# Kernel optimization log

Measured on AMD Instinct MI355X. Metric: run time of the kernel, lower is better.

The kernel has to match this reference:

```python
import jax, jax.numpy as jnp
import numpy as np

EPS = 1e-5

def layernorm(x, g, b):
    mu = jnp.mean(x, axis=-1, keepdims=True)
    var = jnp.mean(jnp.square(x - mu), axis=-1, keepdims=True)
    return (x - mu) * jax.lax.rsqrt(var + EPS) * g + b

def setup_inputs() -> dict:
    key = jax.random.key(0)
    ks = jax.random.split(key, 12)
    B, T, C, H = 4, 2048, 1024, 8
    Dh = C // H          # 128
    Dff = 4 * C          # 4096
    s = 0.02
    return {
        "x":     jax.random.normal(ks[0], (B, T, C), jnp.float32),
        "wq":    jax.random.normal(ks[1], (H, C, Dh), jnp.float32) * s,
        "wk":    jax.random.normal(ks[2], (H, C, Dh), jnp.float32) * s,
        "wv":    jax.random.normal(ks[3], (H, C, Dh), jnp.float32) * s,
        "w1":    jax.random.normal(ks[4], (C, Dff), jnp.float32) * s,
        "b1":    jnp.zeros((Dff,), jnp.float32),
        "w2":    jax.random.normal(ks[5], (Dff, C), jnp.float32) * s,
        "b2":    jnp.zeros((C,), jnp.float32),
        "ln1_g": jnp.ones((C,), jnp.float32),
        "ln1_b": jnp.zeros((C,), jnp.float32),
        "ln2_g": jnp.ones((C,), jnp.float32),
        "ln2_b": jnp.zeros((C,), jnp.float32),
    }

def reference(x, wq, wk, wv, w1, b1, w2, b2, ln1_g, ln1_b, ln2_g, ln2_b):
    B, T, C = x.shape
    H, _, Dh = wq.shape
    # --- multi-head self-attention (pre-LN) ---
    h = layernorm(x, ln1_g, ln1_b)
    q = jnp.einsum("btc,hcd->bhtd", h, wq)
    k = jnp.einsum("btc,hcd->bhtd", h, wk)
    v = jnp.einsum("btc,hcd->bhtd", h, wv)
    # NOTE: original multiplies by sqrt(head_size) (not divide) -- kept faithful
    scores = jnp.einsum("bhtd,bhsd->bhts", q, k) * (Dh ** 0.5)
    attn = jax.nn.softmax(scores, axis=-1)
    # dropout(p=0.2) treated as identity (eval mode)
    o = jnp.einsum("bhts,bhsd->bhtd", attn, v)
    # concat heads along last dim: head h fills contiguous slice
    o = o.transpose(0, 2, 1, 3).reshape(B, T, H * Dh)
    x = x + o  # no output projection in original module
    # --- feed-forward (pre-LN) ---
    h2 = layernorm(x, ln2_g, ln2_b)
    ff = jax.nn.relu(h2 @ w1 + b1) @ w2 + b2
    return x + ff
```

## Files before the change

kernel.cpp:

```cpp
#include <hip/hip_runtime.h>
#include <hip/hip_bf16.h>
#include <math.h>

#define B_   4
#define T_   2048
#define C_   1024
#define H_   8
#define DH   128
#define DFF  4096
#define M_   (B_*T_)

typedef __attribute__((ext_vector_type(8))) short bf16x8;
typedef __attribute__((ext_vector_type(4))) float f32x4;
typedef __attribute__((ext_vector_type(2))) unsigned int u32x2;

#define SC2 16.32223094f

__device__ __forceinline__ unsigned short f2bf(float x) {
  union { float f; unsigned u; } v; v.f = x;
  return (unsigned short)((v.u + 0x7fffu + ((v.u >> 16) & 1u)) >> 16);
}
__device__ __forceinline__ float bf2f(unsigned short h) {
  union { unsigned u; float f; } v; v.u = ((unsigned)h) << 16; return v.f;
}

__device__ __forceinline__ f32x4 mfma_bf16(bf16x8 a, bf16x8 b, f32x4 c) {
  return __builtin_amdgcn_mfma_f32_16x16x32_bf16(a, b, c, 0, 0, 0);
}

__device__ __forceinline__ void gll16(const void* g, void* l) {
  __builtin_amdgcn_global_load_lds((const __attribute__((address_space(1))) void*)g,
                                   (__attribute__((address_space(3))) void*)l,
                                   16, 0, 0);
}

__global__ __launch_bounds__(256) void ln_kernel(const float* __restrict__ in,
                                                 const float* __restrict__ g,
                                                 const float* __restrict__ bb,
                                                 unsigned short* __restrict__ h_hi,
                                                 unsigned short* __restrict__ h_lo) {
  __shared__ float red[8];
  const int row = blockIdx.x;
  const int tid = threadIdx.x;
  const float* p = in + (size_t)row * C_;
  const float4 xv = *(const float4*)(p + (tid << 2));
  float s  = xv.x + xv.y + xv.z + xv.w;
  float sq = xv.x*xv.x + xv.y*xv.y + xv.z*xv.z + xv.w*xv.w;
  #pragma unroll
  for (int off = 32; off > 0; off >>= 1) {
    s  += __shfl_xor(s, off);
    sq += __shfl_xor(sq, off);
  }
  if ((tid & 63) == 0) { red[(tid >> 6) * 2] = s; red[(tid >> 6) * 2 + 1] = sq; }
  __syncthreads();
  s  = red[0] + red[2] + red[4] + red[6];
  sq = red[1] + red[3] + red[5] + red[7];
  const float mu  = s * (1.0f / C_);
  const float var = sq * (1.0f / C_) - mu * mu;
  const float rs  = rsqrtf(var + 1e-5f);
  const float4 gv = *(const float4*)(g  + (tid << 2));
  const float4 bv = *(const float4*)(bb + (tid << 2));
  float ov[4];
  ov[0] = (xv.x - mu) * rs * gv.x + bv.x;
  ov[1] = (xv.y - mu) * rs * gv.y + bv.y;
  ov[2] = (xv.z - mu) * rs * gv.z + bv.z;
  ov[3] = (xv.w - mu) * rs * gv.w + bv.w;
  ushort4 hv, lv;
  unsigned short* hp = (unsigned short*)&hv;
  unsigned short* lp = (unsigned short*)&lv;
  #pragma unroll
  for (int j = 0; j < 4; ++j) {
    hp[j] = f2bf(ov[j]);
    lp[j] = f2bf(ov[j] - bf2f(hp[j]));
  }
  *(ushort4*)(h_hi + (size_t)row * C_ + (tid << 2)) = hv;
  *(ushort4*)(h_lo + (size_t)row * C_ + (tid << 2)) = lv;
}

__global__ __launch_bounds__(256) void cvt_t_kernel(const float* __restrict__ in,
                                                    unsigned short* __restrict__ out,
                                                    int R, int CC) {
  __shared__ float tile[32][33];
  const int r0 = blockIdx.y << 5, c0 = blockIdx.x << 5;
  const int tr = threadIdx.x >> 3, tc4 = (threadIdx.x & 7) << 2;
  const float4 vv = *(const float4*)(in + (size_t)(r0 + tr) * CC + c0 + tc4);
  tile[tr][tc4+0] = vv.x; tile[tr][tc4+1] = vv.y;
  tile[tr][tc4+2] = vv.z; tile[tr][tc4+3] = vv.w;
  __syncthreads();
  ushort4 o;
  o.x = f2bf(tile[tc4+0][tr]); o.y = f2bf(tile[tc4+1][tr]);
  o.z = f2bf(tile[tc4+2][tr]); o.w = f2bf(tile[tc4+3][tr]);
  *(ushort4*)(out + (size_t)(c0 + tr) * R + r0 + tc4) = o;
}

__global__ __launch_bounds__(256) void cvt_qkv_kernel(const float* __restrict__ wq,
                                                      const float* __restrict__ wk,
                                                      const float* __restrict__ wv,
                                                      unsigned short* __restrict__ wt_hi,
                                                      unsigned short* __restrict__ wt_lo) {
  const int z = blockIdx.z;
  const int which = z >> 3, head = z & 7;
  const float* in = (which == 0 ? wq : (which == 1 ? wk : wv)) + (size_t)head * C_ * DH;
  unsigned short* oh = wt_hi + (size_t)z * DH * C_;
  unsigned short* ol = wt_lo + (size_t)z * DH * C_;
  __shared__ float tile[32][33];
  const int r0 = blockIdx.y << 5, c0 = blockIdx.x << 5;
  const int tr = threadIdx.x >> 3, tc4 = (threadIdx.x & 7) << 2;
  const float4 vv = *(const float4*)(in + (size_t)(r0 + tr) * DH + c0 + tc4);
  tile[tr][tc4+0] = vv.x; tile[tr][tc4+1] = vv.y;
  tile[tr][tc4+2] = vv.z; tile[tr][tc4+3] = vv.w;
  __syncthreads();
  ushort4 hv, lv;
  unsigned short* hp = (unsigned short*)&hv;
  unsigned short* lp = (unsigned short*)&lv;
  #pragma unroll
  for (int j = 0; j < 4; ++j) {
    const float val = tile[tc4+j][tr];
    hp[j] = f2bf(val);
    lp[j] = f2bf(val - bf2f(hp[j]));
  }
  *(ushort4*)(oh + (size_t)(c0 + tr) * C_ + r0 + tc4) = hv;
  *(ushort4*)(ol + (size_t)(c0 + tr) * C_ + r0 + tc4) = lv;
}


__device__ __forceinline__ void gemm128_split3(
    const unsigned short* __restrict__ Ah, const unsigned short* __restrict__ Al,
    int lda,
    const unsigned short* __restrict__ Bh, const unsigned short* __restrict__ Bl,
    int ldb, int K, f32x4 (&acc)[4][4],
    unsigned short* AhS, unsigned short* AlS,
    unsigned short* BhS, unsigned short* BlS) {
  const int tid  = threadIdx.x;
  const int w    = tid >> 6;
  const int lane = tid & 63;
  const int l15  = lane & 15, quad = lane >> 4;
  const int srow = lane >> 2;
  const int skc  = ((lane & 3) << 3) ^ (((srow >> 1) & 3) << 3);
  const int wm = w & 1, wn = w >> 1;
  const int ro = ((quad ^ ((l15 >> 1) & 3)) << 3);

  for (int k0 = 0; k0 < K; k0 += 32) {
    __syncthreads();
    #pragma unroll
    for (int i = 0; i < 2; ++i) {
      const int seg  = w * 2 + i;
      const int r    = seg * 16 + srow;
      const int lofs = seg * 512 + lane * 8;
      gll16(Ah + (size_t)r * lda + k0 + skc, AhS + lofs);
      gll16(Bh + (size_t)r * ldb + k0 + skc, BhS + lofs);
      gll16(Al + (size_t)r * lda + k0 + skc, AlS + lofs);
      gll16(Bl + (size_t)r * ldb + k0 + skc, BlS + lofs);
    }
    __syncthreads();
    bf16x8 aH[4], bH[4], aL[4], bL[4];
    #pragma unroll
    for (int t = 0; t < 4; ++t) {
      aH[t] = *(const bf16x8*)&AhS[(wm * 64 + t * 16 + l15) * 32 + ro];
      bH[t] = *(const bf16x8*)&BhS[(wn * 64 + t * 16 + l15) * 32 + ro];
      aL[t] = *(const bf16x8*)&AlS[(wm * 64 + t * 16 + l15) * 32 + ro];
      bL[t] = *(const bf16x8*)&BlS[(wn * 64 + t * 16 + l15) * 32 + ro];
    }
    #pragma unroll
    for (int rt = 0; rt < 4; ++rt)
      #pragma unroll
      for (int ct = 0; ct < 4; ++ct) {
        acc[rt][ct] = mfma_bf16(aL[rt], bH[ct], acc[rt][ct]);
        acc[rt][ct] = mfma_bf16(aH[rt], bL[ct], acc[rt][ct]);
        acc[rt][ct] = mfma_bf16(aH[rt], bH[ct], acc[rt][ct]);
      }
  }
}

__device__ __forceinline__ void gemm128_db(
    const unsigned short* __restrict__ Ah, int lda,
    const unsigned short* __restrict__ Bh, int ldb, int K, f32x4 (&acc)[4][4],
    unsigned short (&AS0)[4096], unsigned short (&AS1)[4096],
    unsigned short (&BS0)[4096], unsigned short (&BS1)[4096]) {
  const int tid  = threadIdx.x;
  const int w    = tid >> 6;
  const int lane = tid & 63;
  const int l15  = lane & 15, quad = lane >> 4;
  const int srow = lane >> 2;
  const int skc  = ((lane & 3) << 3) ^ (((srow >> 1) & 3) << 3);
  const int wm = w & 1, wn = w >> 1;
  const int ro = ((quad ^ ((l15 >> 1) & 3)) << 3);
  const int Km = K - 1;

  auto STG = [&](int k0, unsigned short* A, unsigned short* B) {
    #pragma unroll
    for (int i = 0; i < 2; ++i) {
      const int seg  = w * 2 + i;
      const int r    = seg * 16 + srow;
      const int lofs = seg * 512 + lane * 8;
      gll16(Ah + (size_t)r * lda + k0 + skc, A + lofs);
      gll16(Bh + (size_t)r * ldb + k0 + skc, B + lofs);
    }
  };
  auto CMP = [&](const unsigned short* A, const unsigned short* B) {
    bf16x8 aH[4], bH[4];
    #pragma unroll
    for (int t = 0; t < 4; ++t) {
      aH[t] = *(const bf16x8*)&A[(wm * 64 + t * 16 + l15) * 32 + ro];
      bH[t] = *(const bf16x8*)&B[(wn * 64 + t * 16 + l15) * 32 + ro];
    }
    #pragma unroll
    for (int rt = 0; rt < 4; ++rt)
      #pragma unroll
      for (int ct = 0; ct < 4; ++ct)
        acc[rt][ct] = mfma_bf16(aH[rt], bH[ct], acc[rt][ct]);
  };

  STG(0, AS0, BS0);
  for (int k0 = 0; k0 < K; k0 += 64) {
    __syncthreads();
    STG((k0 + 32) & Km, AS1, BS1);
    CMP(AS0, BS0);
    __syncthreads();
    STG((k0 + 64) & Km, AS0, BS0);
    CMP(AS1, BS1);
  }
}

__global__ __launch_bounds__(256) void qkm_kernel(const unsigned short* __restrict__ h_hi,
                                                  const unsigned short* __restrict__ h_lo,
                                                  const unsigned short* __restrict__ wt_hi,
                                                  const unsigned short* __restrict__ wt_lo,
                                                  unsigned short* __restrict__ q_hi,
                                                  unsigned short* __restrict__ q_lo,
                                                  unsigned short* __restrict__ k_hi,
                                                  unsigned short* __restrict__ k_lo) {
  __shared__ __align__(16) unsigned short AhS[4096], AlS[4096];
  __shared__ __align__(16) unsigned short BhS[4096], BlS[4096];
  const int m0 = blockIdx.x << 7;
  const int z  = blockIdx.y;
  const int which = z >> 3, head = z & 7;
  f32x4 acc[4][4];
  #pragma unroll
  for (int i = 0; i < 4; ++i)
    #pragma unroll
    for (int j = 0; j < 4; ++j)
      #pragma unroll
      for (int r = 0; r < 4; ++r) acc[i][j][r] = 0.f;
  gemm128_split3(h_hi + (size_t)m0 * C_, h_lo + (size_t)m0 * C_, C_,
                 wt_hi + (size_t)z * DH * C_, wt_lo + (size_t)z * DH * C_, C_,
                 C_, acc, AhS, AlS, BhS, BlS);
  const int lane = threadIdx.x & 63, w = threadIdx.x >> 6;
  const int l15 = lane & 15, quad = lane >> 4;
  const int wm = w & 1, wn = w >> 1;
  const int bh = (m0 >> 11) * H_ + head;
  const int tbase = (m0 & (T_ - 1)) + wm * 64 + quad * 4;
  if (which == 0) {
    #pragma unroll
    for (int rt = 0; rt < 4; ++rt)
      #pragma unroll
      for (int ct = 0; ct < 4; ++ct) {
        const int d = wn * 64 + ct * 16 + l15;
        #pragma unroll
        for (int r = 0; r < 4; ++r) {
          const int t = tbase + rt * 16 + r;
          const float val = acc[rt][ct][r] * SC2;
          const unsigned short hb = f2bf(val);
          const size_t idx = ((size_t)bh * T_ + t) * DH + d;
          q_hi[idx] = hb;
          q_lo[idx] = f2bf(val - bf2f(hb));
        }
      }
  } else {
    #pragma unroll
    for (int rt = 0; rt < 4; ++rt)
      #pragma unroll
      for (int ct = 0; ct < 4; ++ct) {
        const int d = wn * 64 + ct * 16 + l15;
        #pragma unroll
        for (int r = 0; r < 4; ++r) {
          const int t = tbase + rt * 16 + r;
          const int tt = t & 31;
          const float val = acc[rt][ct][r];
          const unsigned short hb = f2bf(val);
          const size_t idx = (((size_t)bh * 64 + (t >> 5)) * 4 + (d >> 5)) * 1024
                           + (size_t)tt * 32 + ((d & 31) ^ (((tt >> 1) & 3) << 3));
          k_hi[idx] = hb;
          k_lo[idx] = f2bf(val - bf2f(hb));
        }
      }
  }
}

__global__ __launch_bounds__(256) void vm_kernel(const unsigned short* __restrict__ h_hi,
                                                 const unsigned short* __restrict__ wv_hi,
                                                 unsigned short* __restrict__ vimg) {
  __shared__ __align__(16) unsigned short AS0[4096], AS1[4096];
  __shared__ __align__(16) unsigned short BS0[4096], BS1[4096];
  const int m0 = blockIdx.x << 7;
  const int head = blockIdx.y;
  f32x4 acc[4][4];
  #pragma unroll
  for (int i = 0; i < 4; ++i)
    #pragma unroll
    for (int j = 0; j < 4; ++j)
      #pragma unroll
      for (int r = 0; r < 4; ++r) acc[i][j][r] = 0.f;
  gemm128_db(h_hi + (size_t)m0 * C_, C_,
             wv_hi + (size_t)(16 + head) * DH * C_, C_,
             C_, acc, AS0, AS1, BS0, BS1);
  const int lane = threadIdx.x & 63, w = threadIdx.x >> 6;
  const int l15 = lane & 15, quad = lane >> 4;
  const int wm = w & 1, wn = w >> 1;
  const int bh = (m0 >> 11) * H_ + head;
  #pragma unroll
  for (int rt = 0; rt < 4; ++rt)
    #pragma unroll
    for (int ct = 0; ct < 4; ++ct) {
      const int d  = wn * 64 + ct * 16 + l15;
      const int t0 = (m0 & (T_ - 1)) + wm * 64 + rt * 16 + quad * 4;
      const int key = (t0 & 31) ^ (((d >> 1) & 3) << 3);
      ushort4 pk;
      pk.x = f2bf(acc[rt][ct][0]); pk.y = f2bf(acc[rt][ct][1]);
      pk.z = f2bf(acc[rt][ct][2]); pk.w = f2bf(acc[rt][ct][3]);
      *(ushort4*)&vimg[(((size_t)bh * 64 + (t0 >> 5)) * 128 + d) * 32 + key] = pk;
    }
}

__global__ __launch_bounds__(256) void ff1_kernel(const unsigned short* __restrict__ h2,
                                                  const unsigned short* __restrict__ w1t,
                                                  const float* __restrict__ b1,
                                                  unsigned short* __restrict__ ff1) {
  __shared__ __align__(16) unsigned short AS0[4096], AS1[4096];
  __shared__ __align__(16) unsigned short BS0[4096], BS1[4096];
  const int n0 = blockIdx.x << 7;
  const int m0 = blockIdx.y << 7;
  f32x4 acc[4][4];
  #pragma unroll
  for (int i = 0; i < 4; ++i)
    #pragma unroll
    for (int j = 0; j < 4; ++j)
      #pragma unroll
      for (int r = 0; r < 4; ++r) acc[i][j][r] = 0.f;
  gemm128_db(h2 + (size_t)m0 * C_, C_,
             w1t + (size_t)n0 * C_, C_,
             C_, acc, AS0, AS1, BS0, BS1);
  const int lane = threadIdx.x & 63, w = threadIdx.x >> 6;
  const int l15 = lane & 15, quad = lane >> 4;
  const int wm = w & 1, wn = w >> 1;
  #pragma unroll
  for (int rt = 0; rt < 4; ++rt)
    #pragma unroll
    for (int ct = 0; ct < 4; ++ct) {
      const int n = n0 + wn * 64 + ct * 16 + l15;
      const float bias = b1[n];
      #pragma unroll
      for (int r = 0; r < 4; ++r) {
        const int m = m0 + wm * 64 + rt * 16 + quad * 4 + r;
        ff1[(size_t)m * DFF + n] = f2bf(fmaxf(acc[rt][ct][r] + bias, 0.f));
      }
    }
}

__global__ __launch_bounds__(256) void ff2_kernel(const unsigned short* __restrict__ ff1,
                                                  const unsigned short* __restrict__ w2t,
                                                  const float* __restrict__ b2,
                                                  const float* __restrict__ xo,
                                                  float* __restrict__ out) {
  __shared__ __align__(16) unsigned short AS0[4096], AS1[4096];
  __shared__ __align__(16) unsigned short BS0[4096], BS1[4096];
  const int n0 = blockIdx.x << 7;
  const int m0 = blockIdx.y << 7;
  f32x4 acc[4][4];
  #pragma unroll
  for (int i = 0; i < 4; ++i)
    #pragma unroll
    for (int j = 0; j < 4; ++j)
      #pragma unroll
      for (int r = 0; r < 4; ++r) acc[i][j][r] = 0.f;
  gemm128_db(ff1 + (size_t)m0 * DFF, DFF,
             w2t + (size_t)n0 * DFF, DFF,
             DFF, acc, AS0, AS1, BS0, BS1);
  const int lane = threadIdx.x & 63, w = threadIdx.x >> 6;
  const int l15 = lane & 15, quad = lane >> 4;
  const int wm = w & 1, wn = w >> 1;
  #pragma unroll
  for (int rt = 0; rt < 4; ++rt)
    #pragma unroll
    for (int ct = 0; ct < 4; ++ct) {
      const int n = n0 + wn * 64 + ct * 16 + l15;
      const float bias = b2[n];
      #pragma unroll
      for (int r = 0; r < 4; ++r) {
        const int m = m0 + wm * 64 + rt * 16 + quad * 4 + r;
        out[(size_t)m * C_ + n] = acc[rt][ct][r] + bias + xo[(size_t)m * C_ + n];
      }
    }
}

#define BQ 128

__global__ __launch_bounds__(512, 4) void attn_kernel(
    const unsigned short* __restrict__ q_hi, const unsigned short* __restrict__ q_lo,
    const unsigned short* __restrict__ k_hi, const unsigned short* __restrict__ k_lo,
    const unsigned short* __restrict__ vimg,
    const float* __restrict__ x, float* __restrict__ xo) {
  __shared__ __align__(16) unsigned short Kh0[4096], Kh1[4096];
  __shared__ __align__(16) unsigned short Kl0[4096], Kl1[4096];
  __shared__ __align__(16) unsigned short Vt0[8192], Vt1[8192];

  const int bid   = blockIdx.x + (T_ / BQ) * blockIdx.y;
  const int chunk = bid >> 3;
  const int bh    = (bid & 7) * 4 + (chunk >> 4);
  const int qt0   = (chunk & 15) * BQ;

  const int tid  = threadIdx.x;
  const int w    = tid >> 6;
  const int lane = tid & 63;
  const int l15  = lane & 15;
  const int quad = lane >> 4;
  const int swz  = (l15 >> 1) & 3;
  const int srcbase = quad * 20;
  const int sA   = ((quad & 1) << 5) + l15;
  const int sB   = sA + 16;
  const int bsel = (quad >> 1) & 1;

  bf16x8 Qh[4], Ql[4];
  {
    const int row = qt0 + w * 16 + l15;
    #pragma unroll
    for (int kc = 0; kc < 4; ++kc) {
      const size_t off = ((size_t)bh * T_ + row) * DH + kc * 32 + quad * 8;
      Qh[kc] = *(const bf16x8*)(q_hi + off);
      Ql[kc] = *(const bf16x8*)(q_lo + off);
    }
  }

  f32x4 O[8];
  #pragma unroll
  for (int n = 0; n < 8; ++n)
    #pragma unroll
    for (int r = 0; r < 4; ++r) O[n][r] = 0.f;
  float m_cur = -1e30f;
  float l_cur = 0.f;

  auto STAGE_K = [&](int kt, unsigned short* KH, unsigned short* KL) {
    const size_t tb = ((size_t)bh * 64 + kt) * 4096;
    const int ofs = w * 512 + lane * 8;
    gll16(k_hi + tb + ofs, KH + ofs);
    gll16(k_lo + tb + ofs, KL + ofs);
  };
  auto STAGE_V = [&](int jv, unsigned short* VT) {
    const size_t tb = ((size_t)bh * 64 + jv * 2) * 4096;
    #pragma unroll
    for (int i = 0; i < 2; ++i) {
      const int o = (w * 2 + i) * 512 + lane * 8;
      gll16(vimg + tb + o, VT + o);
    }
  };
  auto QKT = [&](const unsigned short* KH, const unsigned short* KL, f32x4* Sp) {
    __builtin_amdgcn_s_setprio(1);
    #pragma unroll
    for (int kc = 0; kc < 4; ++kc)
      #pragma unroll
      for (int ct = 0; ct < 2; ++ct) {
        const int o = kc * 1024 + (ct * 16 + l15) * 32 + ((quad ^ swz) << 3);
        const bf16x8 kh = *(const bf16x8*)&KH[o];
        const bf16x8 kl = *(const bf16x8*)&KL[o];
        Sp[ct] = mfma_bf16(kl, Qh[kc], Sp[ct]);
        Sp[ct] = mfma_bf16(kh, Ql[kc], Sp[ct]);
        Sp[ct] = mfma_bf16(kh, Qh[kc], Sp[ct]);
      }
    __builtin_amdgcn_s_setprio(0);
  };

  STAGE_K(0, Kh0, Kl0);
  STAGE_K(1, Kh1, Kl1);
  STAGE_V(0, Vt0);

  for (int j = 0; j < T_ / 64; ++j) {
    const unsigned short* Vc = (j & 1) ? Vt1 : Vt0;
    unsigned short*       Vn = (j & 1) ? Vt0 : Vt1;

    __syncthreads();
    f32x4 S[4];
    #pragma unroll
    for (int ct = 0; ct < 4; ++ct)
      #pragma unroll
      for (int r = 0; r < 4; ++r) S[ct][r] = 0.f;
    QKT(Kh0, Kl0, &S[0]);
    __syncthreads();
    STAGE_K((2 * j + 2) & 63, Kh0, Kl0);
    STAGE_V((j + 1) & 31, Vn);
    QKT(Kh1, Kl1, &S[2]);
    __syncthreads();
    STAGE_K((2 * j + 3) & 63, Kh1, Kl1);

    float mx = -1e30f;
    #pragma unroll
    for (int ct = 0; ct < 4; ++ct)
      mx = fmaxf(mx, fmaxf(fmaxf(S[ct][0], S[ct][1]), fmaxf(S[ct][2], S[ct][3])));
    mx = fmaxf(mx, __shfl_xor(mx, 16));
    mx = fmaxf(mx, __shfl_xor(mx, 32));

    if (__any(mx > m_cur + 8.f)) {
      const float mn = fmaxf(m_cur, mx);
      const float al = exp2f(m_cur - mn);
      m_cur = mn;
      l_cur *= al;
      #pragma unroll
      for (int r = 0; r < 4; ++r) {
        const float ar = __shfl(al, srcbase + r);
        #pragma unroll
        for (int n = 0; n < 8; ++n) O[n][r] *= ar;
      }
    }

    unsigned pu[8];
    float rs = 0.f;
    #pragma unroll
    for (int ct = 0; ct < 4; ++ct) {
      const float p0 = exp2f(S[ct][0] - m_cur);
      const float p1 = exp2f(S[ct][1] - m_cur);
      const float p2 = exp2f(S[ct][2] - m_cur);
      const float p3 = exp2f(S[ct][3] - m_cur);
      rs += (p0 + p1) + (p2 + p3);
      pu[ct * 2 + 0] = (__float_as_uint(p1) & 0xffff0000u) | (__float_as_uint(p0) >> 16);
      pu[ct * 2 + 1] = (__float_as_uint(p3) & 0xffff0000u) | (__float_as_uint(p2) >> 16);
    }
    rs += __shfl_xor(rs, 16);
    rs += __shfl_xor(rs, 32);
    l_cur += rs;

    bf16x8 aP[2];
    #pragma unroll
    for (int g = 0; g < 2; ++g) {
      const unsigned xA0 = (unsigned)__shfl((int)pu[4 * g + 0], sA);
      const unsigned yA0 = (unsigned)__shfl((int)pu[4 * g + 2], sA);
      const unsigned xA1 = (unsigned)__shfl((int)pu[4 * g + 1], sA);
      const unsigned yA1 = (unsigned)__shfl((int)pu[4 * g + 3], sA);
      const unsigned xB0 = (unsigned)__shfl((int)pu[4 * g + 0], sB);
      const unsigned yB0 = (unsigned)__shfl((int)pu[4 * g + 2], sB);
      const unsigned xB1 = (unsigned)__shfl((int)pu[4 * g + 1], sB);
      const unsigned yB1 = (unsigned)__shfl((int)pu[4 * g + 3], sB);
      union { unsigned u[4]; bf16x8 v; } cv;
      cv.u[0] = bsel ? yA0 : xA0;
      cv.u[1] = bsel ? yA1 : xA1;
      cv.u[2] = bsel ? yB0 : xB0;
      cv.u[3] = bsel ? yB1 : xB1;
      aP[g] = cv.v;
    }

    __builtin_amdgcn_s_setprio(1);
    #pragma unroll
    for (int g = 0; g < 2; ++g)
      #pragma unroll
      for (int n = 0; n < 8; ++n) {
        const bf16x8 bv =
            *(const bf16x8*)&Vc[g * 4096 + (n * 16 + l15) * 32 + ((quad ^ swz) << 3)];
        O[n] = mfma_bf16(aP[g], bv, O[n]);
      }
    __builtin_amdgcn_s_setprio(0);
  }

  const int b = bh >> 3, hh = bh & 7;
  #pragma unroll
  for (int r = 0; r < 4; ++r) {
    const float lr = __shfl(l_cur, srcbase + r);
    const float inv_l = 1.0f / lr;
    const int t = qt0 + w * 16 + quad * 4 + r;
    const size_t xrow = ((size_t)(b * T_ + t)) * C_ + (size_t)hh * DH;
    #pragma unroll
    for (int n = 0; n < 8; ++n) {
      const int d = n * 16 + l15;
      xo[xrow + d] = x[xrow + d] + O[n][r] * inv_l;
    }
  }
}

extern "C" void kernel_launch(void* const* d_in, const int* in_sizes, int n_in,
                              void* d_out, int out_size, void* d_ws, size_t ws_size,
                              hipStream_t stream) {
  (void)in_sizes; (void)n_in; (void)out_size; (void)ws_size;
  const float* x     = (const float*)d_in[0];
  const float* wq    = (const float*)d_in[1];
  const float* wk    = (const float*)d_in[2];
  const float* wv    = (const float*)d_in[3];
  const float* w1    = (const float*)d_in[4];
  const float* b1    = (const float*)d_in[5];
  const float* w2    = (const float*)d_in[6];
  const float* b2    = (const float*)d_in[7];
  const float* ln1_g = (const float*)d_in[8];
  const float* ln1_b = (const float*)d_in[9];
  const float* ln2_g = (const float*)d_in[10];
  const float* ln2_b = (const float*)d_in[11];
  float* out = (float*)d_out;

  char* W = (char*)d_ws;
  float* xo = (float*)(W);
  unsigned short* q_hi  = (unsigned short*)(W + (32u  << 20));
  unsigned short* q_lo  = (unsigned short*)(W + (48u  << 20));
  unsigned short* k_hi  = (unsigned short*)(W + (64u  << 20));
  unsigned short* k_lo  = (unsigned short*)(W + (80u  << 20));
  unsigned short* vimg  = (unsigned short*)(W + (96u  << 20));
  unsigned short* ff1   = (unsigned short*)(W + (32u  << 20));
  unsigned short* h_hi  = (unsigned short*)(W + (112u << 20));
  unsigned short* h_lo  = (unsigned short*)(W + (128u << 20));
  unsigned short* w1t   = (unsigned short*)(W + (144u << 20));
  unsigned short* w2t   = (unsigned short*)(W + (152u << 20));
  unsigned short* wt_hi = (unsigned short*)(W + (160u << 20));
  unsigned short* wt_lo = (unsigned short*)(W + (166u << 20));

  cvt_t_kernel<<<dim3(DFF / 32, C_ / 32), 256, 0, stream>>>(w1, w1t, C_, DFF);
  cvt_t_kernel<<<dim3(C_ / 32, DFF / 32), 256, 0, stream>>>(w2, w2t, DFF, C_);
  cvt_qkv_kernel<<<dim3(DH / 32, C_ / 32, 24), 256, 0, stream>>>(wq, wk, wv, wt_hi, wt_lo);
  ln_kernel<<<M_, 256, 0, stream>>>(x, ln1_g, ln1_b, h_hi, h_lo);
  qkm_kernel<<<dim3(M_ / 128, 16), 256, 0, stream>>>(h_hi, h_lo, wt_hi, wt_lo,
                                                     q_hi, q_lo, k_hi, k_lo);
  vm_kernel<<<dim3(M_ / 128, H_), 256, 0, stream>>>(h_hi, wt_hi, vimg);
  attn_kernel<<<dim3(T_ / BQ, B_ * H_), 512, 0, stream>>>(q_hi, q_lo, k_hi, k_lo,
                                                          vimg, x, xo);
  ln_kernel<<<M_, 256, 0, stream>>>(xo, ln2_g, ln2_b, h_hi, h_lo);
  ff1_kernel<<<dim3(DFF / 128, M_ / 128), 256, 0, stream>>>(h_hi, w1t, b1, ff1);
  ff2_kernel<<<dim3(C_ / 128, M_ / 128), 256, 0, stream>>>(ff1, w2t, b2, xo, out);
}
```

Before: 618.5 us.

## Software-pipeline PV matmul one tile behind QK^T and transpose O accumulator

The attention loop is restructured so each 64-key tile is staged in one step, with K-hi double-buffered and K-lo single-buffered. The P·V MFMA for the previous tile runs after the current QK^T and next-tile loads are issued, which removes one barrier per iteration and overlaps softmax with memory traffic. The PV MFMA operands are swapped so O is held transposed with the query row in l15. That lets the rescale and 1/l factors apply without cross-lane shuffles and allows float4 epilogue loads and stores. The trade-offs are reduced LDS double buffering for K-lo and an extra drain step after the loop.

```diff
diff --git a/kernel.cpp b/kernel.cpp
--- a/kernel.cpp
+++ b/kernel.cpp
@@ -400,9 +400,9 @@
     const unsigned short* __restrict__ k_hi, const unsigned short* __restrict__ k_lo,
     const unsigned short* __restrict__ vimg,
     const float* __restrict__ x, float* __restrict__ xo) {
-  __shared__ __align__(16) unsigned short Kh0[4096], Kh1[4096];
-  __shared__ __align__(16) unsigned short Kl0[4096], Kl1[4096];
-  __shared__ __align__(16) unsigned short Vt0[8192], Vt1[8192];
+  __shared__ __align__(16) unsigned short KhS[2][8192];
+  __shared__ __align__(16) unsigned short KlS[8192];
+  __shared__ __align__(16) unsigned short VtS[2][8192];
 
   const int bid   = blockIdx.x + (T_ / BQ) * blockIdx.y;
   const int chunk = bid >> 3;
@@ -415,7 +415,6 @@
   const int l15  = lane & 15;
   const int quad = lane >> 4;
   const int swz  = (l15 >> 1) & 3;
-  const int srcbase = quad * 20;
   const int sA   = ((quad & 1) << 5) + l15;
   const int sB   = sA + 16;
   const int bsel = (quad >> 1) & 1;
@@ -439,57 +438,73 @@
   float m_cur = -1e30f;
   float l_cur = 0.f;
 
-  auto STAGE_K = [&](int kt, unsigned short* KH, unsigned short* KL) {
-    const size_t tb = ((size_t)bh * 64 + kt) * 4096;
-    const int ofs = w * 512 + lane * 8;
-    gll16(k_hi + tb + ofs, KH + ofs);
-    gll16(k_lo + tb + ofs, KL + ofs);
+  auto STAGE_K64 = [&](int jt) {
+    const size_t tb = ((size_t)bh * 64 + (jt & 31) * 2) * 4096;
+    unsigned short* KH = &KhS[jt & 1][0];
+    const int o = tid * 8;
+    gll16(k_hi + tb + o, KH + o);
+    gll16(k_hi + tb + 4096 + o, KH + 4096 + o);
+    gll16(k_lo + tb + o, KlS + o);
+    gll16(k_lo + tb + 4096 + o, KlS + 4096 + o);
   };
-  auto STAGE_V = [&](int jv, unsigned short* VT) {
-    const size_t tb = ((size_t)bh * 64 + jv * 2) * 4096;
-    #pragma unroll
-    for (int i = 0; i < 2; ++i) {
-      const int o = (w * 2 + i) * 512 + lane * 8;
-      gll16(vimg + tb + o, VT + o);
-    }
+  auto STAGE_V64 = [&](int jt) {
+    const size_t tb = ((size_t)bh * 64 + jt * 2) * 4096;
+    unsigned short* VT = &VtS[jt & 1][0];
+    const int o = tid * 8;
+    gll16(vimg + tb + o, VT + o);
+    gll16(vimg + tb + 4096 + o, VT + 4096 + o);
   };
-  auto QKT = [&](const unsigned short* KH, const unsigned short* KL, f32x4* Sp) {
-    __builtin_amdgcn_s_setprio(1);
-    #pragma unroll
-    for (int kc = 0; kc < 4; ++kc)
-      #pragma unroll
-      for (int ct = 0; ct < 2; ++ct) {
-        const int o = kc * 1024 + (ct * 16 + l15) * 32 + ((quad ^ swz) << 3);
-        const bf16x8 kh = *(const bf16x8*)&KH[o];
-        const bf16x8 kl = *(const bf16x8*)&KL[o];
-        Sp[ct] = mfma_bf16(kl, Qh[kc], Sp[ct]);
-        Sp[ct] = mfma_bf16(kh, Ql[kc], Sp[ct]);
-        Sp[ct] = mfma_bf16(kh, Qh[kc], Sp[ct]);
-      }
-    __builtin_amdgcn_s_setprio(0);
-  };
-
-  STAGE_K(0, Kh0, Kl0);
-  STAGE_K(1, Kh1, Kl1);
-  STAGE_V(0, Vt0);
+
+  bf16x8 bPp[2];
+
+  STAGE_K64(0);
 
   for (int j = 0; j < T_ / 64; ++j) {
-    const unsigned short* Vc = (j & 1) ? Vt1 : Vt0;
-    unsigned short*       Vn = (j & 1) ? Vt0 : Vt1;
-
     __syncthreads();
+
     f32x4 S[4];
     #pragma unroll
     for (int ct = 0; ct < 4; ++ct)
       #pragma unroll
       for (int r = 0; r < 4; ++r) S[ct][r] = 0.f;
-    QKT(Kh0, Kl0, &S[0]);
+    {
+      const unsigned short* KH = &KhS[j & 1][0];
+      __builtin_amdgcn_s_setprio(1);
+      #pragma unroll
+      for (int sub = 0; sub < 2; ++sub)
+        #pragma unroll
+        for (int kc = 0; kc < 4; ++kc)
+          #pragma unroll
+          for (int c2 = 0; c2 < 2; ++c2) {
+            const int o = sub * 4096 + kc * 1024 + (c2 * 16 + l15) * 32
+                        + ((quad ^ swz) << 3);
+            const bf16x8 kh = *(const bf16x8*)&KH[o];
+            const bf16x8 kl = *(const bf16x8*)&KlS[o];
+            f32x4& Sr = S[sub * 2 + c2];
+            Sr = mfma_bf16(kl, Qh[kc], Sr);
+            Sr = mfma_bf16(kh, Ql[kc], Sr);
+            Sr = mfma_bf16(kh, Qh[kc], Sr);
+          }
+      __builtin_amdgcn_s_setprio(0);
+    }
+
     __syncthreads();
-    STAGE_K((2 * j + 2) & 63, Kh0, Kl0);
-    STAGE_V((j + 1) & 31, Vn);
-    QKT(Kh1, Kl1, &S[2]);
-    __syncthreads();
-    STAGE_K((2 * j + 3) & 63, Kh1, Kl1);
+    STAGE_K64(j + 1);
+    STAGE_V64(j);
+
+    if (j > 0) {
+      const unsigned short* VT = &VtS[(j - 1) & 1][0];
+      __builtin_amdgcn_s_setprio(1);
+      #pragma unroll
+      for (int g = 0; g < 2; ++g)
+        #pragma unroll
+        for (int n = 0; n < 8; ++n) {
+          const bf16x8 av =
+              *(const bf16x8*)&VT[g * 4096 + (n * 16 + l15) * 32 + ((quad ^ swz) << 3)];
+          O[n] = mfma_bf16(av, bPp[g], O[n]);
+        }
+      __builtin_amdgcn_s_setprio(0);
+    }
 
     float mx = -1e30f;
     #pragma unroll
@@ -504,11 +519,9 @@
       m_cur = mn;
       l_cur *= al;
       #pragma unroll
-      for (int r = 0; r < 4; ++r) {
-        const float ar = __shfl(al, srcbase + r);
+      for (int n = 0; n < 8; ++n)
         #pragma unroll
-        for (int n = 0; n < 8; ++n) O[n][r] *= ar;
-      }
+        for (int r = 0; r < 4; ++r) O[n][r] *= al;
     }
 
     unsigned pu[8];
@@ -527,7 +540,6 @@
     rs += __shfl_xor(rs, 32);
     l_cur += rs;
 
-    bf16x8 aP[2];
     #pragma unroll
     for (int g = 0; g < 2; ++g) {
       const unsigned xA0 = (unsigned)__shfl((int)pu[4 * g + 0], sA);
@@ -543,33 +555,37 @@
       cv.u[1] = bsel ? yA1 : xA1;
       cv.u[2] = bsel ? yB0 : xB0;
       cv.u[3] = bsel ? yB1 : xB1;
-      aP[g] = cv.v;
-    }
-
-    __builtin_amdgcn_s_setprio(1);
+      bPp[g] = cv.v;
+    }
+  }
+
+  __syncthreads();
+  {
+    const unsigned short* VT = &VtS[(T_ / 64 - 1) & 1][0];
     #pragma unroll
     for (int g = 0; g < 2; ++g)
       #pragma unroll
       for (int n = 0; n < 8; ++n) {
-        const bf16x8 bv =
-            *(const bf16x8*)&Vc[g * 4096 + (n * 16 + l15) * 32 + ((quad ^ swz) << 3)];
-        O[n] = mfma_bf16(aP[g], bv, O[n]);
+        const bf16x8 av =
+            *(const bf16x8*)&VT[g * 4096 + (n * 16 + l15) * 32 + ((quad ^ swz) << 3)];
+        O[n] = mfma_bf16(av, bPp[g], O[n]);
       }
-    __builtin_amdgcn_s_setprio(0);
   }
 
   const int b = bh >> 3, hh = bh & 7;
-  #pragma unroll
-  for (int r = 0; r < 4; ++r) {
-    const float lr = __shfl(l_cur, srcbase + r);
-    const float inv_l = 1.0f / lr;
-    const int t = qt0 + w * 16 + quad * 4 + r;
-    const size_t xrow = ((size_t)(b * T_ + t)) * C_ + (size_t)hh * DH;
-    #pragma unroll
-    for (int n = 0; n < 8; ++n) {
-      const int d = n * 16 + l15;
-      xo[xrow + d] = x[xrow + d] + O[n][r] * inv_l;
-    }
+  const float inv_l = 1.0f / l_cur;
+  const int t = qt0 + w * 16 + l15;
+  const size_t xrow = ((size_t)(b * T_ + t)) * C_ + (size_t)hh * DH;
+  #pragma unroll
+  for (int n = 0; n < 8; ++n) {
+    const int d = n * 16 + quad * 4;
+    const float4 xv = *(const float4*)(x + xrow + d);
+    float4 ov;
+    ov.x = xv.x + O[n][0] * inv_l;
+    ov.y = xv.y + O[n][1] * inv_l;
+    ov.z = xv.z + O[n][2] * inv_l;
+    ov.w = xv.w + O[n][3] * inv_l;
+    *(float4*)(xo + xrow + d) = ov;
   }
 }
 
```

Result: slower. 651.2 us (+5.3%).
